# Performance work log

Hardware: AMD Instinct MI355X
Metric: run time of the kernel (lower is better)

## Reference

```python
import jax, jax.numpy as jnp
import numpy as np

# MUCMA: multiuser CMA adaptive MIMO FIR equalizer (commplax af.mucma)
# framed_signal: (N, taps, dims) complex, carried as re/im float32 pairs.
N, TAPS, DIMS, DELTA = 131072, 19, 2, 6
LR = 2.0 ** (-13)
BETA = 0.999
R2 = 1.32  # E|a|^4 / E|a|^2 for unit-power 16QAM constellation


def setup_inputs() -> dict:
    key = jax.random.key(0)
    k1, k2 = jax.random.split(key)
    fr_re = jax.random.normal(k1, (N, TAPS, DIMS), dtype=jnp.float32) * 0.7071
    fr_im = jax.random.normal(k2, (N, TAPS, DIMS), dtype=jnp.float32) * 0.7071
    # initial MIMO weights: identity at the center tap (commplax mucma init)
    w0_re = np.zeros((DIMS, DIMS, TAPS), dtype=np.float32)
    ctap = (TAPS + 1) // 2 - 1
    w0_re[np.arange(DIMS), np.arange(DIMS), ctap] = 1.0
    return {
        'fr_re': fr_re,
        'fr_im': fr_im,
        'w0_re': jnp.asarray(w0_re),
        'w0_im': jnp.zeros((DIMS, DIMS, TAPS), jnp.float32),
    }


def _mucma_forward(fr_re, fr_im, w0_re, w0_im):
    u_all = fr_re + 1j * fr_im                      # (N, taps, dims) complex64
    w0 = (w0_re + 1j * w0_im).astype(u_all.dtype)   # (dims, dims, taps)
    # mask kills self cross-correlation terms (k == l)
    mask = (1.0 - jnp.eye(DIMS, dtype=jnp.float32))[:, :, None]

    def step(carry, u):
        # u: (taps, dims) frame of input samples
        w, z, r, bp = carry
        v = jnp.einsum('ijt,tj->i', w, u)                     # MIMO FIR output, (dims,)
        z = jnp.concatenate((v[None, :], z[:-1]))             # output delay line, (delta, dims)
        # running cross-correlation r[k,l,d] ~ E[z_k(n) z_l(n-d)^*]
        r = BETA * r + (1.0 - BETA) * jnp.einsum('k,dl->kld', v, z.conj())
        rhat = (r / (1.0 - bp)) * mask                        # bias-corrected, off-diagonal only
        e = R2 - jnp.abs(v) ** 2                              # CMA modulus error, (dims,) real
        loss = jnp.sum(e ** 2) + 2.0 * jnp.sum(jnp.abs(rhat) ** 2)
        uc = u.conj().T[None, :, :]                           # (1, dims, taps)
        g_cma = -2.0 * e[:, None, None] * v[:, None, None] * uc
        g_mu = 2.0 * jnp.einsum('kld,dl->k', rhat, z.conj())[:, None, None] * uc
        w_new = w - LR * (g_cma + g_mu)
        bp = bp * BETA
        # emit the weights USED for this symbol (pre-update), as commplax does
        return (w_new, z, r, bp), (w, loss)

    z0 = jnp.zeros((DELTA, DIMS), u_all.dtype)
    r0 = jnp.zeros((DIMS, DIMS, DELTA), u_all.dtype)
    carry0 = (w0, z0, r0, jnp.float32(BETA))
    _, (ws, _losses) = jax.lax.scan(step, carry0, u_all)
    # apply: per-symbol MIMO filtering with the recorded weight trace
    sig = jnp.einsum('nijt,ntj->ni', ws, u_all)               # (N, dims) complex
    return jnp.stack([sig.real, sig.imag], axis=-1)           # (N, dims, 2) float32


def reference(fr_re, fr_im, w0_re, w0_im):
    return _mucma_forward(fr_re, fr_im, w0_re, w0_im)
```

## Files before the change

kernel.cpp:

```cpp
#include <hip/hip_runtime.h>
#include <stdint.h>


typedef float v2f __attribute__((ext_vector_type(2)));
typedef float v4f __attribute__((ext_vector_type(4), aligned(8)));

constexpr int   NTAPS   = 19;
constexpr int   FRST    = 38;
constexpr float BETA_C  = 0.999f;
constexpr float OMB_C   = 0.001f;
constexpr float LR_C    = 0.0001220703125f;
constexpr float R2_C    = 1.32f;
constexpr int   SPLIT_N = 24576;

template <int CTRL>
__device__ __forceinline__ float dpp_add(float x) {
    return x + __int_as_float(__builtin_amdgcn_update_dpp(
        0, __float_as_int(x), CTRL, 0xF, 0xF, true));
}
template <int CTRL>
__device__ __forceinline__ float dpp_mov(float x) {
    return __int_as_float(__builtin_amdgcn_update_dpp(
        0, __float_as_int(x), CTRL, 0xF, 0xF, true));
}
__device__ __forceinline__ float rowred_bcast(float x) {
    x = dpp_add<0x121>(x);
    x = dpp_add<0x122>(x);
    x = dpp_add<0x124>(x);
    x = dpp_add<0x128>(x);
    return x;
}
__device__ __forceinline__ void plane32_swap(float& a, float& b) {
    asm("s_nop 1\n\t"
        "v_permlane32_swap_b32 %0, %1\n\t"
        "s_nop 1"
        : "+v"(a), "+v"(b));
}
__device__ __forceinline__ void plane32_swap2(float& a, float& b, float& c, float& d) {
    asm("s_nop 1\n\t"
        "v_permlane32_swap_b32 %0, %1\n\t"
        "v_permlane32_swap_b32 %2, %3\n\t"
        "s_nop 1"
        : "+v"(a), "+v"(b), "+v"(c), "+v"(d));
}
__device__ __forceinline__ void wg_barrier() {
    asm volatile("s_waitcnt lgkmcnt(0)\n\ts_barrier" ::: "memory");
}

__global__ void __launch_bounds__(64)
gram7_kernel(const float* __restrict__ fr_re, const float* __restrict__ fr_im,
             float* __restrict__ sc, int nsym)
{
    __shared__ float lre[71 * FRST], lim[71 * FRST];
    const int lane = threadIdx.x;
    const int n0   = blockIdx.x * 64;
    const int base = (n0 - 7) * FRST;
    const long gmax = (long)nsym * FRST;
    for (int idx = lane; idx < 71 * FRST; idx += 64) {
        const long g = (long)base + idx;
        float a = 0.f, b = 0.f;
        if (g >= 0 && g < gmax) { a = fr_re[g]; b = fr_im[g]; }
        lre[idx] = a; lim[idx] = b;
    }
    __syncthreads();
    const int m = n0 + lane;
    if (m >= nsym) return;
    const float* br = lre + (lane + 7) * FRST;
    const float* bi = lim + (lane + 7) * FRST;
    float out[16];
#pragma unroll
    for (int k = 1; k <= 7; ++k) {
        const float* ar = br - k * FRST;
        const float* ai = bi - k * FRST;
        float sr = 0.f, si = 0.f;
#pragma unroll
        for (int e = 0; e < FRST; ++e) {
            sr = fmaf(ar[e], br[e], fmaf(ai[e], bi[e], sr));
            si = fmaf(-ai[e], br[e], fmaf(ar[e], bi[e], si));
        }
        const bool ok = (m >= k);
        out[2*(k-1)]   = ok ? sr : 0.f;
        out[2*(k-1)+1] = ok ? si : 0.f;
    }
    out[14] = 0.f; out[15] = 0.f;
    float* d = sc + (size_t)m * 16;
#pragma unroll
    for (int j = 0; j < 4; ++j)
        *(v4f*)(d + 4*j) = (v4f){out[4*j], out[4*j+1], out[4*j+2], out[4*j+3]};
}

struct A_St {
    float acr[8], aci[8];
    float histr[8], histi[8];
    v4f   scr[4][4];
    float z_re, z_im, r_re, r_im, bp;
};
struct A_Ctx {
    const float* scp; float* outp;
    float (*aring)[2][32][2]; float (*cring)[2][32][2];
    int h, sl; bool d0f, csel; int last;
};

template <int S, bool EARLY, bool TAIL>
__device__ __forceinline__ void a_pos(A_St& st, const A_Ctx& c, int SB)
{
    constexpr int s8 = S & 7, s4 = S & 3, NC = 4 + (S & 3);
    const int m = SB + S;

    float vr = st.acr[s8], vi = st.aci[s8];
#pragma unroll
    for (int k = 1; k <= NC; ++k) {
        const float hr = st.histr[(S - k) & 7];
        const float hi = st.histi[(S - k) & 7];
        const v4f sv = st.scr[s4][(k - 1) >> 1];
        const float Sr = (k & 1) ? sv.x : sv.z;
        const float Si = (k & 1) ? sv.y : sv.w;
        vr = fmaf(-hr, Sr, fmaf( hi, Si, vr));
        vi = fmaf(-hr, Si, fmaf(-hi, Sr, vi));
    }

    *(v2f*)(c.outp + 4 * (size_t)m + 2 * c.h) = (v2f){vr, vi};

    float Xr = vr, Yr = vr, Xi = vi, Yi = vi;
    plane32_swap2(Xr, Yr, Xi, Yi);
    const float vlr = c.csel ? Xr : Yr;
    const float vli = c.csel ? Xi : Yi;

    const float zsr = dpp_mov<0x111>(st.z_re);
    const float zsi = dpp_mov<0x111>(st.z_im);
    st.z_re = c.d0f ? vlr : zsr;
    st.z_im = c.d0f ? vli : zsi;

    const float ar = OMB_C * vr, ai = OMB_C * vi;
    st.r_re = BETA_C * st.r_re + (ar * st.z_re + ai * st.z_im);
    st.r_im = BETA_C * st.r_im + (ai * st.z_re - ar * st.z_im);

    float qr = st.r_re * st.z_re + st.r_im * st.z_im;
    float qi = st.r_im * st.z_re - st.r_re * st.z_im;
    qr = rowred_bcast(qr);
    qi = rowred_bcast(qi);

    float i2;
    if (EARLY) {
        const float inv = __builtin_amdgcn_rcpf(1.0f - st.bp);
        st.bp *= BETA_C;
        i2 = (2.0f * LR_C) * inv;
    } else {
        i2 = 2.0f * LR_C;
    }
    const float t  = vr * vr + vi * vi;
    const float e2 = fmaf(2.0f * LR_C, t, -(2.0f * LR_C) * R2_C);
    const float cr = fmaf(e2, vr, i2 * qr);
    const float ci = fmaf(e2, vi, i2 * qi);

    st.histr[s8] = cr; st.histi[s8] = ci;
    *(v2f*)&c.cring[s8][c.h][c.sl][0] = (v2f){cr, ci};

    int mp = m + 4;
    if (TAIL) { if (mp > c.last) mp = c.last; }
    const float* p = c.scp + (size_t)mp * 16;
#pragma unroll
    for (int j = 0; j < 4; ++j)
        st.scr[s4][j] = *(const v4f*)(p + 4 * j);
}

template <int I, bool EARLY, bool TAIL>
__device__ __forceinline__ void a_sub(A_St& st, const A_Ctx& c, int SB)
{
#pragma unroll
    for (int t = 0; t < 4; ++t) {
        const v2f a0 = *(const v2f*)&c.aring[(4*I + t) & 7][c.h][0][0];
        st.acr[(4*I + t) & 7] = a0.x;
        st.aci[(4*I + t) & 7] = a0.y;
    }
    a_pos<4*I + 0, EARLY, TAIL>(st, c, SB);
    a_pos<4*I + 1, EARLY, TAIL>(st, c, SB);
    a_pos<4*I + 2, EARLY, TAIL>(st, c, SB);
    a_pos<4*I + 3, EARLY, TAIL>(st, c, SB);
    wg_barrier();
}
template <bool EARLY, bool TAIL>
__device__ __forceinline__ void a_super(A_St& st, const A_Ctx& c, int SB)
{
    a_sub<0, EARLY, TAIL>(st, c, SB);
    a_sub<1, EARLY, TAIL>(st, c, SB);
    a_sub<2, EARLY, TAIL>(st, c, SB);
    a_sub<3, EARLY, TAIL>(st, c, SB);
}

struct B_St {
    v2f wA_r, wA_i, wB_r, wB_i;
    v4f ur[16], ui[16];
    float mA, mB;
};
struct B_Ctx {
    const float* pre; const float* pim;
    float (*aring)[2][32][2]; float (*cring)[2][32][2];
    int h, sl; int last;
};

__device__ __forceinline__ v2f b_tree(const B_St& s, const v4f& uR, const v4f& uI) {
    const v2f uA_r = {uR.x,uR.y}, uB_r = {uR.z,uR.w};
    const v2f uA_i = {uI.x,uI.y}, uB_i = {uI.z,uI.w};
    v2f tr = s.wA_r*uA_r - s.wA_i*uA_i + s.wB_r*uB_r - s.wB_i*uB_i;
    v2f ti = s.wA_r*uA_i + s.wA_i*uA_r + s.wB_r*uB_i + s.wB_i*uB_r;
    return (v2f){ rowred_bcast(tr.x + tr.y), rowred_bcast(ti.x + ti.y) };
}

template <int I, bool TAIL>
__device__ __forceinline__ void b_sub(B_St& st, const B_Ctx& c, int SB)
{
    float ccr[4], cci[4];
#pragma unroll
    for (int t = 0; t < 4; ++t) {
        const v2f cc = *(const v2f*)&c.cring[(4*I + 4 + t) & 7][c.h][0][0];
        ccr[t] = cc.x; cci[t] = cc.y;
    }
#pragma unroll
    for (int t = 0; t < 4; ++t) {
        const float crA = ccr[t] * st.mA, ciA = cci[t] * st.mA;
        const float crB = ccr[t] * st.mB, ciB = cci[t] * st.mB;
        const v4f uR = st.ur[(4*I + 12 + t) & 15], uI = st.ui[(4*I + 12 + t) & 15];
        const v2f uA_r = {uR.x,uR.y}, uB_r = {uR.z,uR.w};
        const v2f uA_i = {uI.x,uI.y}, uB_i = {uI.z,uI.w};
        st.wA_r -= (v2f){crA,crA}*uA_r + (v2f){ciA,ciA}*uA_i;
        st.wA_i -= (v2f){ciA,ciA}*uA_r - (v2f){crA,crA}*uA_i;
        st.wB_r -= (v2f){crB,crB}*uB_r + (v2f){ciB,ciB}*uB_i;
        st.wB_i -= (v2f){ciB,ciB}*uB_r - (v2f){crB,crB}*uB_i;
    }
#pragma unroll
    for (int t = 0; t < 4; ++t) {
        const v2f T = b_tree(st, st.ur[(4*I + 4 + t) & 15], st.ui[(4*I + 4 + t) & 15]);
        *(v2f*)&c.aring[(4*I + 4 + t) & 7][c.h][c.sl][0] = T;
    }
#pragma unroll
    for (int t = 0; t < 4; ++t) {
        int f = SB + 4*I + 8 + t;
        if (TAIL) { if (f > c.last) f = c.last; }
        st.ur[(4*I + 8 + t) & 15] = *(const v4f*)(c.pre + (size_t)f * FRST);
        st.ui[(4*I + 8 + t) & 15] = *(const v4f*)(c.pim + (size_t)f * FRST);
    }
    wg_barrier();
}
template <bool TAIL>
__device__ __forceinline__ void b_super(B_St& st, const B_Ctx& c, int SB)
{
    b_sub<0, TAIL>(st, c, SB);
    b_sub<1, TAIL>(st, c, SB);
    b_sub<2, TAIL>(st, c, SB);
    b_sub<3, TAIL>(st, c, SB);
}

__global__ void __launch_bounds__(128, 1)
__attribute__((amdgpu_waves_per_eu(1, 1)))
mucma2b_kernel(const float* __restrict__ fr_re, const float* __restrict__ fr_im,
               const float* __restrict__ w0r_in, const float* __restrict__ w0i_in,
               const float* __restrict__ scp, float* __restrict__ outp, int nsym)
{
    __shared__ __align__(16) float cring[8][2][32][2];
    __shared__ __align__(16) float aring[8][2][32][2];

    const int  tid  = threadIdx.x;
    const int  wid  = tid >> 6;
    const int  lane = tid & 63;
    const int  sl   = lane & 31;
    const int  h    = lane >> 5;
    const int  loff = (4*sl < 34) ? 4*sl : 34;
    const int  last = nsym - 1;
    const int  SBend = nsym - 16;

    bool csel;
    { const float own = h ? 11.f : 7.f; float v = own, X = own;
      plane32_swap(X, v); csel = (X != own); }

    if (wid == 0) {
        A_St st; A_Ctx c;
        c.scp = scp; c.outp = outp; c.aring = aring; c.cring = cring;
        c.h = h; c.sl = sl; c.d0f = ((sl & 15) == 10); c.csel = csel; c.last = last;
#pragma unroll
        for (int k = 0; k < 8; ++k) {
            st.histr[k] = 0.f; st.histi[k] = 0.f;
            st.acr[k] = 0.f;  st.aci[k] = 0.f;
        }
        st.z_re = 0.f; st.z_im = 0.f; st.r_re = 0.f; st.r_im = 0.f; st.bp = BETA_C;
#pragma unroll
        for (int s = 0; s < 4; ++s)
#pragma unroll
            for (int j = 0; j < 4; ++j)
                st.scr[s][j] = *(const v4f*)(scp + (size_t)s * 16 + 4 * j);
        if (lane < 32) cring[lane >> 2][(lane >> 1) & 1][0][lane & 1] = 0.f;
        wg_barrier();

        int SB = 0;
        for (; SB < SPLIT_N; SB += 16) a_super<true , false>(st, c, SB);
        for (; SB < SBend;   SB += 16) a_super<false, false>(st, c, SB);
        a_super<false, true>(st, c, SB);
    } else {
        B_St st; B_Ctx c;
        c.pre = fr_re + loff; c.pim = fr_im + loff;
        c.aring = aring; c.cring = cring; c.h = h; c.sl = sl; c.last = last;
        st.mA = (sl <= 8) ? 1.f : 0.f;
        st.mB = (sl <= 9) ? 1.f : 0.f;
        st.wA_r = (v2f){0.f,0.f}; st.wA_i = (v2f){0.f,0.f};
        st.wB_r = (v2f){0.f,0.f}; st.wB_i = (v2f){0.f,0.f};
        if (sl <= 8) {
            const int b = h*FRST + 2*sl;
            st.wA_r.x = w0r_in[b];       st.wA_r.y = w0r_in[b+NTAPS];
            st.wA_i.x = w0i_in[b];       st.wA_i.y = w0i_in[b+NTAPS];
            st.wB_r.x = w0r_in[b+1];     st.wB_r.y = w0r_in[b+NTAPS+1];
            st.wB_i.x = w0i_in[b+1];     st.wB_i.y = w0i_in[b+NTAPS+1];
        } else if (sl == 9) {
            st.wB_r.x = w0r_in[h*FRST+18];  st.wB_r.y = w0r_in[h*FRST+37];
            st.wB_i.x = w0i_in[h*FRST+18];  st.wB_i.y = w0i_in[h*FRST+37];
        }
#pragma unroll
        for (int k = 0; k < 12; ++k) {
            st.ur[k] = *(const v4f*)(c.pre + (size_t)k * FRST);
            st.ui[k] = *(const v4f*)(c.pim + (size_t)k * FRST);
        }
#pragma unroll
        for (int k = 12; k < 16; ++k) {
            st.ur[k] = (v4f){0.f,0.f,0.f,0.f};
            st.ui[k] = (v4f){0.f,0.f,0.f,0.f};
        }
#pragma unroll
        for (int t = 0; t < 4; ++t) {
            const v2f T = b_tree(st, st.ur[t], st.ui[t]);
            *(v2f*)&aring[t][h][sl][0] = T;
        }
        wg_barrier();

        int SB = 0;
        for (; SB < SBend; SB += 16) b_super<false>(st, c, SB);
        b_super<true>(st, c, SB);
    }
}

__global__ void __launch_bounds__(64, 1)
__attribute__((amdgpu_waves_per_eu(1, 1)))
mucma_scan_fb(const float* __restrict__ fr_re, const float* __restrict__ fr_im,
              const float* __restrict__ w0r_in, const float* __restrict__ w0i_in,
              float* __restrict__ out, int nsym)
{
    const int  lane = threadIdx.x;
    const int  sl   = lane & 31;
    const int  h    = lane >> 5;
    const int  loff = (4 * sl < 34) ? 4 * sl : 34;
    const float mA  = (sl <= 8) ? 1.f : 0.f;
    const float mB  = (sl <= 9) ? 1.f : 0.f;
    const bool d0f  = (sl == 10);
    const bool stfl = (sl == 0);

    v2f wA_r = {0.f,0.f}, wA_i = {0.f,0.f}, wB_r = {0.f,0.f}, wB_i = {0.f,0.f};
    if (sl <= 8) {
        const int b = h * FRST + 2 * sl;
        wA_r.x = w0r_in[b];         wA_r.y = w0r_in[b + NTAPS];
        wA_i.x = w0i_in[b];         wA_i.y = w0i_in[b + NTAPS];
        wB_r.x = w0r_in[b + 1];     wB_r.y = w0r_in[b + NTAPS + 1];
        wB_i.x = w0i_in[b + 1];     wB_i.y = w0i_in[b + NTAPS + 1];
    } else if (sl == 9) {
        wB_r.x = w0r_in[h * FRST + 18];  wB_r.y = w0r_in[h * FRST + 37];
        wB_i.x = w0i_in[h * FRST + 18];  wB_i.y = w0i_in[h * FRST + 37];
    }
    float r_re = 0.f, r_im = 0.f, z_re = 0.f, z_im = 0.f;
    float bp = BETA_C;

    bool csel;
    {
        const float own = h ? 11.f : 7.f;
        float v = own, X = own;
        plane32_swap(X, v);
        csel = (X != own);
    }

    const float* pre = fr_re + loff;
    const float* pim = fr_im + loff;

    v4f rr[8], ri[8];
#pragma unroll
    for (int p = 0; p < 8; ++p) {
        const int idx = (p < nsym) ? p : (nsym - 1);
        rr[p] = *(const v4f*)(pre + (size_t)idx * FRST);
        ri[p] = *(const v4f*)(pim + (size_t)idx * FRST);
    }

    auto body = [&](int n, int p, int npf) {
        const v4f uR = rr[p], uI = ri[p];
        rr[p] = *(const v4f*)(pre + (size_t)npf * FRST);
        ri[p] = *(const v4f*)(pim + (size_t)npf * FRST);

        const v2f uA_r = {uR.x, uR.y}, uB_r = {uR.z, uR.w};
        const v2f uA_i = {uI.x, uI.y}, uB_i = {uI.z, uI.w};

        v2f tr = wA_r * uA_r - wA_i * uA_i + wB_r * uB_r - wB_i * uB_i;
        v2f ti = wA_r * uA_i + wA_i * uA_r + wB_r * uB_i + wB_i * uB_r;
        float xr = rowred_bcast(tr.x + tr.y);
        float xi = rowred_bcast(ti.x + ti.y);
        const float vkr = xr, vki = xi;

        float Xr = xr, Xi = xi;
        plane32_swap(Xr, xr);
        plane32_swap(Xi, xi);
        const float vlr = csel ? Xr : xr;
        const float vli = csel ? Xi : xi;

        const float zsr = dpp_mov<0x111>(z_re);
        const float zsi = dpp_mov<0x111>(z_im);
        z_re = d0f ? vlr : zsr;
        z_im = d0f ? vli : zsi;

        const float ar = OMB_C * vkr, ai = OMB_C * vki;
        r_re = BETA_C * r_re + (ar * z_re + ai * z_im);
        r_im = BETA_C * r_im + (ai * z_re - ar * z_im);

        float qr = r_re * z_re + r_im * z_im;
        float qi = r_im * z_re - r_re * z_im;
        qr = rowred_bcast(qr);
        qi = rowred_bcast(qi);

        const float inv = __builtin_amdgcn_rcpf(1.0f - bp);
        bp *= BETA_C;
        const float i2 = (2.0f * LR_C) * inv;
        const float ek = R2_C - (vkr * vkr + vki * vki);
        const float e2 = (-2.0f * LR_C) * ek;
        const float cr = e2 * vkr + i2 * qr;
        const float ci = e2 * vki + i2 * qi;

        const float crA = cr * mA, ciA = ci * mA;
        const float crB = cr * mB, ciB = ci * mB;
        wA_r -= (v2f){crA,crA} * uA_r + (v2f){ciA,ciA} * uA_i;
        wA_i -= (v2f){ciA,ciA} * uA_r - (v2f){crA,crA} * uA_i;
        wB_r -= (v2f){crB,crB} * uB_r + (v2f){ciB,ciB} * uB_i;
        wB_i -= (v2f){ciB,ciB} * uB_r - (v2f){crB,crB} * uB_i;

        if (stfl) {
            v2f o; o.x = vkr; o.y = vki;
            *(v2f*)(out + 4 * (size_t)n + 2 * h) = o;
        }
    };

    int NBmain = nsym / 8 - 1;
    if (NBmain < 0) NBmain = 0;
    for (int b = 0; b < NBmain; ++b) {
        const int nb = b * 8;
#pragma unroll
        for (int p = 0; p < 8; ++p) body(nb + p, p, nb + p + 8);
    }
    for (int nb = NBmain * 8; nb < nsym; nb += 8) {
#pragma unroll
        for (int p = 0; p < 8; ++p) {
            const int n = nb + p;
            if (n < nsym) {
                int npf = n + 8;
                if (npf > nsym - 1) npf = nsym - 1;
                body(n, p, npf);
            }
        }
    }
}

extern "C" void kernel_launch(void* const* d_in, const int* in_sizes, int n_in,
                              void* d_out, int out_size, void* d_ws, size_t ws_size,
                              hipStream_t stream)
{
    const float* fr_re = (const float*)d_in[0];
    const float* fr_im = (const float*)d_in[1];
    const float* w0r   = (const float*)d_in[2];
    const float* w0i   = (const float*)d_in[3];
    float* outp = (float*)d_out;
    const int nsym = in_sizes[0] / FRST;

    const bool use2 = (nsym % 16 == 0) && (nsym >= SPLIT_N + 16)
                   && (ws_size >= (size_t)nsym * 64);
    if (use2) {
        hipLaunchKernelGGL(gram7_kernel, dim3((nsym + 63) / 64), dim3(64), 0, stream,
                           fr_re, fr_im, (float*)d_ws, nsym);
        hipLaunchKernelGGL(mucma2b_kernel, dim3(1), dim3(128), 0, stream,
                           fr_re, fr_im, w0r, w0i, (const float*)d_ws, outp, nsym);
    } else {
        hipLaunchKernelGGL(mucma_scan_fb, dim3(1), dim3(64), 0, stream,
                           fr_re, fr_im, w0r, w0i, outp, nsym);
    }
}
```

Measured before the change: 27.04 ms.

## Precompute next-step history correction and split lag-0 correlation off the serial path

Restructures the per-symbol serial recurrence in the A wave. The history-correction sum for the next symbol is now computed ahead of time from the older terms, leaving only the most recent term on the dependent chain. The lag-0 cross-correlation term is kept in separate registers so that the z delay-line shift can move after the correction is produced. This shortens the latency-bound critical path of the sequential scan, at the cost of a few extra registers and some added arithmetic per step.

```diff
diff --git a/kernel.cpp b/kernel.cpp
--- a/kernel.cpp
+++ b/kernel.cpp
@@ -93,53 +93,54 @@
     float acr[8], aci[8];
     float histr[8], histi[8];
     v4f   scr[4][4];
-    float z_re, z_im, r_re, r_im, bp;
+    float pp_r, pp_i;
+    float z_re, z_im;
+    float r_re, r_im;
+    float r0_r, r0_i;
+    float bp;
 };
 struct A_Ctx {
     const float* scp; float* outp;
     float (*aring)[2][32][2]; float (*cring)[2][32][2];
-    int h, sl; bool d0f, csel; int last;
+    int h, sl; bool d1f, csel; int last;
 };
 
 template <int S, bool EARLY, bool TAIL>
 __device__ __forceinline__ void a_pos(A_St& st, const A_Ctx& c, int SB)
 {
-    constexpr int s8 = S & 7, s4 = S & 3, NC = 4 + (S & 3);
+    constexpr int s8 = S & 7, s4 = S & 3;
+    constexpr int SN = S + 1, s4n = SN & 3, NCn = 4 + (SN & 3);
     const int m = SB + S;
 
-    float vr = st.acr[s8], vi = st.aci[s8];
-#pragma unroll
-    for (int k = 1; k <= NC; ++k) {
-        const float hr = st.histr[(S - k) & 7];
-        const float hi = st.histi[(S - k) & 7];
-        const v4f sv = st.scr[s4][(k - 1) >> 1];
-        const float Sr = (k & 1) ? sv.x : sv.z;
-        const float Si = (k & 1) ? sv.y : sv.w;
-        vr = fmaf(-hr, Sr, fmaf( hi, Si, vr));
-        vi = fmaf(-hr, Si, fmaf(-hi, Sr, vi));
-    }
+    const float h1r = st.histr[(S + 7) & 7];
+    const float h1i = st.histi[(S + 7) & 7];
+    const v4f  sv1 = st.scr[s4][0];
+    float vr = st.acr[s8] + st.pp_r;
+    float vi = st.aci[s8] + st.pp_i;
+    vr = fmaf(-h1r, sv1.x, fmaf( h1i, sv1.y, vr));
+    vi = fmaf(-h1r, sv1.y, fmaf(-h1i, sv1.x, vi));
 
     *(v2f*)(c.outp + 4 * (size_t)m + 2 * c.h) = (v2f){vr, vi};
+
+    const float ar = OMB_C * vr, ai = OMB_C * vi;
+    st.r_re = BETA_C * st.r_re + (ar * st.z_re + ai * st.z_im);
+    st.r_im = BETA_C * st.r_im + (ai * st.z_re - ar * st.z_im);
+    float qr = st.r_re * st.z_re + st.r_im * st.z_im;
+    float qi = st.r_im * st.z_re - st.r_re * st.z_im;
+    qr = rowred_bcast(qr);
+    qi = rowred_bcast(qi);
 
     float Xr = vr, Yr = vr, Xi = vi, Yi = vi;
     plane32_swap2(Xr, Yr, Xi, Yi);
     const float vlr = c.csel ? Xr : Yr;
     const float vli = c.csel ? Xi : Yi;
-
-    const float zsr = dpp_mov<0x111>(st.z_re);
-    const float zsi = dpp_mov<0x111>(st.z_im);
-    st.z_re = c.d0f ? vlr : zsr;
-    st.z_im = c.d0f ? vli : zsi;
-
-    const float ar = OMB_C * vr, ai = OMB_C * vi;
-    st.r_re = BETA_C * st.r_re + (ar * st.z_re + ai * st.z_im);
-    st.r_im = BETA_C * st.r_im + (ai * st.z_re - ar * st.z_im);
-
-    float qr = st.r_re * st.z_re + st.r_im * st.z_im;
-    float qi = st.r_im * st.z_re - st.r_re * st.z_im;
-    qr = rowred_bcast(qr);
-    qi = rowred_bcast(qi);
-
+    st.r0_r = BETA_C * st.r0_r + (ar * vlr + ai * vli);
+    st.r0_i = BETA_C * st.r0_i + (ai * vlr - ar * vli);
+    const float q0r = st.r0_r * vlr + st.r0_i * vli;
+    const float q0i = st.r0_i * vlr - st.r0_r * vli;
+
+    const float qtr = qr + q0r;
+    const float qti = qi + q0i;
     float i2;
     if (EARLY) {
         const float inv = __builtin_amdgcn_rcpf(1.0f - st.bp);
@@ -148,13 +149,39 @@
     } else {
         i2 = 2.0f * LR_C;
     }
-    const float t  = vr * vr + vi * vi;
-    const float e2 = fmaf(2.0f * LR_C, t, -(2.0f * LR_C) * R2_C);
-    const float cr = fmaf(e2, vr, i2 * qr);
-    const float ci = fmaf(e2, vi, i2 * qi);
+    const float tt = vr * vr + vi * vi;
+    const float e2 = fmaf(2.0f * LR_C, tt, -(2.0f * LR_C) * R2_C);
+    const float cr = fmaf(e2, vr, i2 * qtr);
+    const float ci = fmaf(e2, vi, i2 * qti);
 
     st.histr[s8] = cr; st.histi[s8] = ci;
     *(v2f*)&c.cring[s8][c.h][c.sl][0] = (v2f){cr, ci};
+
+    const float zsr = dpp_mov<0x111>(st.z_re);
+    const float zsi = dpp_mov<0x111>(st.z_im);
+    st.z_re = c.d1f ? vlr : zsr;
+    st.z_im = c.d1f ? vli : zsi;
+
+    {
+        float p0r = 0.f, p0i = 0.f, p1r = 0.f, p1i = 0.f;
+#pragma unroll
+        for (int k = 2; k <= NCn; ++k) {
+            const float hr = st.histr[(SN - k) & 7];
+            const float hi = st.histi[(SN - k) & 7];
+            const v4f sv = st.scr[s4n][(k - 1) >> 1];
+            const float Sr = (k & 1) ? sv.x : sv.z;
+            const float Si = (k & 1) ? sv.y : sv.w;
+            if (k & 1) {
+                p0r = fmaf(-hr, Sr, fmaf( hi, Si, p0r));
+                p0i = fmaf(-hr, Si, fmaf(-hi, Sr, p0i));
+            } else {
+                p1r = fmaf(-hr, Sr, fmaf( hi, Si, p1r));
+                p1i = fmaf(-hr, Si, fmaf(-hi, Sr, p1i));
+            }
+        }
+        st.pp_r = p0r + p1r;
+        st.pp_i = p0i + p1i;
+    }
 
     int mp = m + 4;
     if (TAIL) { if (mp > c.last) mp = c.last; }
@@ -253,7 +280,7 @@
 
 __global__ void __launch_bounds__(128, 1)
 __attribute__((amdgpu_waves_per_eu(1, 1)))
-mucma2b_kernel(const float* __restrict__ fr_re, const float* __restrict__ fr_im,
+mucma2e_kernel(const float* __restrict__ fr_re, const float* __restrict__ fr_im,
                const float* __restrict__ w0r_in, const float* __restrict__ w0i_in,
                const float* __restrict__ scp, float* __restrict__ outp, int nsym)
 {
@@ -276,13 +303,17 @@
     if (wid == 0) {
         A_St st; A_Ctx c;
         c.scp = scp; c.outp = outp; c.aring = aring; c.cring = cring;
-        c.h = h; c.sl = sl; c.d0f = ((sl & 15) == 10); c.csel = csel; c.last = last;
+        c.h = h; c.sl = sl; c.d1f = ((sl & 15) == 11); c.csel = csel; c.last = last;
 #pragma unroll
         for (int k = 0; k < 8; ++k) {
             st.histr[k] = 0.f; st.histi[k] = 0.f;
             st.acr[k] = 0.f;  st.aci[k] = 0.f;
         }
-        st.z_re = 0.f; st.z_im = 0.f; st.r_re = 0.f; st.r_im = 0.f; st.bp = BETA_C;
+        st.pp_r = 0.f; st.pp_i = 0.f;
+        st.z_re = 0.f; st.z_im = 0.f;
+        st.r_re = 0.f; st.r_im = 0.f;
+        st.r0_r = 0.f; st.r0_i = 0.f;
+        st.bp = BETA_C;
 #pragma unroll
         for (int s = 0; s < 4; ++s)
 #pragma unroll
@@ -337,7 +368,6 @@
 }
 
 __global__ void __launch_bounds__(64, 1)
-__attribute__((amdgpu_waves_per_eu(1, 1)))
 mucma_scan_fb(const float* __restrict__ fr_re, const float* __restrict__ fr_im,
               const float* __restrict__ w0r_in, const float* __restrict__ w0i_in,
               float* __restrict__ out, int nsym)
@@ -475,7 +505,7 @@
     if (use2) {
         hipLaunchKernelGGL(gram7_kernel, dim3((nsym + 63) / 64), dim3(64), 0, stream,
                            fr_re, fr_im, (float*)d_ws, nsym);
-        hipLaunchKernelGGL(mucma2b_kernel, dim3(1), dim3(128), 0, stream,
+        hipLaunchKernelGGL(mucma2e_kernel, dim3(1), dim3(128), 0, stream,
                            fr_re, fr_im, w0r, w0i, (const float*)d_ws, outp, nsym);
     } else {
         hipLaunchKernelGGL(mucma_scan_fb, dim3(1), dim3(64), 0, stream,
```

Result: slower. 28.73 ms (+6.2%).
